# Kernel optimization log

Measured on AMD Instinct MI355X. Metric: run time of the kernel, lower is better.

## Reference

```python
import jax, jax.numpy as jnp
import numpy as np

ATOM_FDIM = 133
BOND_FDIM = 14
DIM = 512
DEPTH = 4
N_ATOMS = 100000
N_BONDS = 300000
MAX_NB = 6
N_MOLS = 500


def _lin(x, w, b):
    return x @ w + b


def setup_inputs() -> dict:
    key = jax.random.key(0)
    ks = jax.random.split(key, 16)
    s = 0.02
    f_atoms = jax.random.normal(ks[0], (N_ATOMS, ATOM_FDIM), jnp.float32)
    f_bonds = jax.random.normal(ks[1], (N_BONDS, BOND_FDIM), jnp.float32)
    a2a = jax.random.randint(ks[2], (N_ATOMS, MAX_NB), 0, N_ATOMS, jnp.int32)
    a2b = jax.random.randint(ks[3], (N_ATOMS, MAX_NB), 0, N_BONDS, jnp.int32)
    # atom 0 is padding -> assign out-of-range segment id so segment_sum drops it
    ids = np.minimum((np.arange(N_ATOMS) - 1) // ((N_ATOMS - 1) // N_MOLS), N_MOLS - 1)
    ids[0] = N_MOLS
    mol_ids = jnp.asarray(ids, jnp.int32)
    return {
        'f_atoms': f_atoms, 'f_bonds': f_bonds, 'a2a': a2a, 'a2b': a2b,
        'mol_ids': mol_ids, 'n_mols': N_MOLS,
        'W_i_w': jax.random.normal(ks[4], (ATOM_FDIM, DIM), jnp.float32) * s,
        'W_i_b': jnp.zeros((DIM,), jnp.float32),
        'Wh0_w': jax.random.normal(ks[5], (DIM + BOND_FDIM, DIM), jnp.float32) * s,
        'Wh0_b': jnp.zeros((DIM,), jnp.float32),
        'Wh1_w': jax.random.normal(ks[6], (DIM, DIM), jnp.float32) * s,
        'Wh1_b': jnp.zeros((DIM,), jnp.float32),
        'Wh2_w': jax.random.normal(ks[7], (DIM, DIM), jnp.float32) * s,
        'Wh2_b': jnp.zeros((DIM,), jnp.float32),
        'Wah0_w': jax.random.normal(ks[8], (ATOM_FDIM, DIM), jnp.float32) * s,
        'Wah0_b': jnp.zeros((DIM,), jnp.float32),
        'Wah1_w': jax.random.normal(ks[9], (DIM, DIM), jnp.float32) * s,
        'Wah1_b': jnp.zeros((DIM,), jnp.float32),
        'Wah2_w': jax.random.normal(ks[10], (DIM, DIM), jnp.float32) * s,
        'Wah2_b': jnp.zeros((DIM,), jnp.float32),
        'W_o_w': jax.random.normal(ks[11], (2 * DIM, DIM), jnp.float32) * s,
        'W_o_b': jnp.zeros((DIM,), jnp.float32),
    }


def reference(f_atoms, f_bonds, a2a, a2b, mol_ids, n_mols,
              W_i_w, W_i_b, Wh0_w, Wh0_b, Wh1_w, Wh1_b, Wh2_w, Wh2_b,
              Wah0_w, Wah0_b, Wah1_w, Wah1_b, Wah2_w, Wah2_b, W_o_w, W_o_b):
    # input atom hidden; row 0 is padding and is zeroed
    h0 = jax.nn.relu(_lin(f_atoms, W_i_w, W_i_b))        # [A, dim]
    msg = h0.at[0].set(0.0)
    self_msg = msg
    # NOTE: original code shares one modulList across all W_h{i} -> shared weights per depth
    nei_bond_sum = jnp.sum(f_bonds[a2b], axis=1)          # [A, BOND_FDIM] (constant over depths)
    for _ in range(DEPTH):
        nei_atom_sum = jnp.sum(msg[a2a], axis=1)          # [A, dim]
        m = jnp.concatenate([nei_atom_sum, nei_bond_sum], axis=1)  # [A, dim+BOND_FDIM]
        m = _lin(jax.nn.relu(m), Wh0_w, Wh0_b)
        m = _lin(jax.nn.relu(m), Wh1_w, Wh1_b)
        m = _lin(jax.nn.relu(m), Wh2_w, Wh2_b)
        m = self_msg + m
        self_msg = m                                      # kept BEFORE zeroing row 0 (as in torch)
        msg = m.at[0].set(0.0)
    a_message = jnp.sum(msg[a2a], axis=1)                 # [A, dim]
    cc = jax.nn.relu(_lin(f_atoms, Wah0_w, Wah0_b))
    cc = jax.nn.relu(_lin(cc, Wah1_w, Wah1_b))
    cc = jax.nn.relu(_lin(cc, Wah2_w, Wah2_b))
    a_input = jnp.concatenate([cc, a_message], axis=1)    # [A, 2*dim]
    out = jax.nn.relu(_lin(a_input, W_o_w, W_o_b))        # [A, dim]
    # per-molecule sum pooling (a_scope); padding atom has id == n_mols -> dropped
    return jax.ops.segment_sum(out, mol_ids, num_segments=n_mols)
```

## Files before the change

kernel.cpp:

```cpp
#include <hip/hip_runtime.h>
#include <stdint.h>
#include <stddef.h>

typedef __attribute__((ext_vector_type(8))) _Float16 half8;
typedef __attribute__((ext_vector_type(4))) float f32x4;

__device__ __forceinline__ void gload_lds16(const void* g, void* l) {
  __builtin_amdgcn_global_load_lds(
      (const __attribute__((address_space(1))) unsigned int*)g,
      (__attribute__((address_space(3))) unsigned int*)l, 16, 0, 0);
}

enum { EPI_RELU = 0, EPI_INIT = 1, EPI_DEPTH = 2 };

template <int EPI, bool SPLIT, bool ATOMS>
__global__ __launch_bounds__(256) void gemm128(
    const void* __restrict__ A1v, int lda1,
    const _Float16* __restrict__ A2, int lda2, int ksplit,
    const _Float16* __restrict__ Bt,
    const float* __restrict__ bias,
    int M, int K,
    _Float16* __restrict__ out_h, int ldo,
    const _Float16* __restrict__ self_h,
    float* self0,
    _Float16* msg_out,
    int row0)
{
  __shared__ __align__(16) _Float16 Alds[128 * 32];
  __shared__ __align__(16) _Float16 Blds[128 * 32];

  const int t = threadIdx.x;
  const int m0 = blockIdx.x * 128;
  const int n0 = blockIdx.y * 128;

  f32x4 acc[4][4];
#pragma unroll
  for (int i = 0; i < 4; ++i)
#pragma unroll
    for (int j = 0; j < 4; ++j) acc[i][j] = (f32x4){0.f, 0.f, 0.f, 0.f};

  const int lane = t & 63;
  const int w = t >> 6;
  const int wr = (w >> 1) * 64;
  const int wc = (w & 1) * 64;
  const int l16 = lane & 15;
  const int quad = lane >> 4;

  for (int kk = 0; kk < K; kk += 32) {
    __syncthreads();
    if (ATOMS) {
      const float* Af = (const float*)A1v;
#pragma unroll
      for (int h = 0; h < 2; ++h) {
        int i = t + h * 256;
        int r = i >> 2, kg = i & 3;
        int row = m0 + r; if (row > M - 1) row = M - 1;
        int k = kk + kg * 8;
        const float* src = Af + (size_t)row * lda1;
        half8 hv;
#pragma unroll
        for (int e = 0; e < 8; ++e) {
          int kc = k + e;
          hv[e] = (_Float16)(kc < ksplit ? src[kc] : 0.f);
        }
        *(half8*)&Alds[i * 8] = hv;
      }
    } else {
      const _Float16* A1 = (const _Float16*)A1v;
#pragma unroll
      for (int h = 0; h < 2; ++h) {
        int i = t + h * 256;
        int r = i >> 2, kg = i & 3;
        int row = m0 + r; if (row > M - 1) row = M - 1;
        int k = kk + kg * 8;
        const _Float16* src;
        if (SPLIT) {
          src = (k < ksplit) ? (A1 + (size_t)row * lda1 + k)
                             : (A2 + (size_t)row * lda2 + (k - ksplit));
        } else {
          src = A1 + (size_t)row * lda1 + k;
        }
        gload_lds16(src, &Alds[i * 8]);
      }
    }
#pragma unroll
    for (int h = 0; h < 2; ++h) {
      int i = t + h * 256;
      int n = i >> 2, kg = i & 3;
      gload_lds16(Bt + (size_t)(n0 + n) * K + kk + kg * 8, &Blds[i * 8]);
    }
    __syncthreads();

    half8 af[4], bf[4];
#pragma unroll
    for (int mi = 0; mi < 4; ++mi)
      af[mi] = *(const half8*)&Alds[(wr + mi * 16 + l16) * 32 + quad * 8];
#pragma unroll
    for (int ni = 0; ni < 4; ++ni)
      bf[ni] = *(const half8*)&Blds[(wc + ni * 16 + l16) * 32 + quad * 8];
#pragma unroll
    for (int mi = 0; mi < 4; ++mi)
#pragma unroll
      for (int ni = 0; ni < 4; ++ni)
        acc[mi][ni] = __builtin_amdgcn_mfma_f32_16x16x32_f16(af[mi], bf[ni], acc[mi][ni], 0, 0, 0);
  }

#pragma unroll
  for (int mi = 0; mi < 4; ++mi) {
#pragma unroll
    for (int ni = 0; ni < 4; ++ni) {
      int col = n0 + wc + ni * 16 + l16;
      float b = bias[col];
#pragma unroll
      for (int r = 0; r < 4; ++r) {
        int row = m0 + wr + mi * 16 + quad * 4 + r;
        if (row < M) {
          float v = acc[mi][ni][r] + b;
          if (EPI == EPI_RELU) {
            v = fmaxf(v, 0.f);
            out_h[(size_t)row * ldo + col] = (_Float16)v;
          } else if (EPI == EPI_INIT) {
            v = fmaxf(v, 0.f);
            if (row == row0) { msg_out[(size_t)row * 512 + col] = (_Float16)0.f; self0[col] = 0.f; }
            else msg_out[(size_t)row * 512 + col] = (_Float16)v;
          } else {
            float self = (row == row0) ? self0[col]
                                       : (float)self_h[(size_t)row * 512 + col];
            v += self;
            if (row == row0) { self0[col] = v; msg_out[(size_t)row * 512 + col] = (_Float16)0.f; }
            else msg_out[(size_t)row * 512 + col] = (_Float16)v;
          }
        }
      }
    }
  }
}

template <bool SPLIT>
__global__ __launch_bounds__(256) void gemm_wide(
    const _Float16* __restrict__ A1, int lda1,
    const _Float16* __restrict__ A2, int lda2, int ksplit,
    const _Float16* __restrict__ Bt, const float* __restrict__ bias,
    int M, int K,
    _Float16* __restrict__ out_h)
{
  __shared__ __align__(16) _Float16 Alds[64 * 32];
  __shared__ __align__(16) _Float16 Blds[512 * 32];
  const int t = threadIdx.x;
  const int m0 = blockIdx.x * 64;
  f32x4 acc[4][8];
#pragma unroll
  for (int i = 0; i < 4; ++i)
#pragma unroll
    for (int j = 0; j < 8; ++j) acc[i][j] = (f32x4){0.f, 0.f, 0.f, 0.f};
  const int lane = t & 63;
  const int w = t >> 6;
  const int wc = w * 128;
  const int l16 = lane & 15;
  const int quad = lane >> 4;
  for (int kk = 0; kk < K; kk += 32) {
    __syncthreads();
    {
      int r = t >> 2, kg = t & 3;
      int row = m0 + r; if (row > M - 1) row = M - 1;
      int k = kk + kg * 8;
      const _Float16* src;
      if (SPLIT) {
        src = (k < ksplit) ? (A1 + (size_t)row * lda1 + k)
                           : (A2 + (size_t)row * lda2 + (k - ksplit));
      } else {
        src = A1 + (size_t)row * lda1 + k;
      }
      gload_lds16(src, &Alds[t * 8]);
    }
#pragma unroll
    for (int h = 0; h < 8; ++h) {
      int i = t + h * 256;
      int n = i >> 2, kg = i & 3;
      gload_lds16(Bt + (size_t)n * K + kk + kg * 8, &Blds[i * 8]);
    }
    __syncthreads();
    half8 af[4], bf[8];
#pragma unroll
    for (int mi = 0; mi < 4; ++mi)
      af[mi] = *(const half8*)&Alds[(mi * 16 + l16) * 32 + quad * 8];
#pragma unroll
    for (int ni = 0; ni < 8; ++ni)
      bf[ni] = *(const half8*)&Blds[(wc + ni * 16 + l16) * 32 + quad * 8];
#pragma unroll
    for (int mi = 0; mi < 4; ++mi)
#pragma unroll
      for (int ni = 0; ni < 8; ++ni)
        acc[mi][ni] = __builtin_amdgcn_mfma_f32_16x16x32_f16(af[mi], bf[ni], acc[mi][ni], 0, 0, 0);
  }
#pragma unroll
  for (int mi = 0; mi < 4; ++mi) {
#pragma unroll
    for (int ni = 0; ni < 8; ++ni) {
      int col = wc + ni * 16 + l16;
      float b = bias[col];
#pragma unroll
      for (int r = 0; r < 4; ++r) {
        int row = m0 + mi * 16 + quad * 4 + r;
        if (row < M) {
          float v = fmaxf(acc[mi][ni][r] + b, 0.f);
          out_h[(size_t)row * 512 + col] = (_Float16)v;
        }
      }
    }
  }
}

template <bool RELU>
__global__ __launch_bounds__(256) void gather_k(
    const _Float16* __restrict__ msg, const int* __restrict__ a2a,
    _Float16* __restrict__ out, int rows)
{
  int t = threadIdx.x;
  int a = blockIdx.x * 4 + (t >> 6);
  if (a >= rows) return;
  int g = t & 63;
  const _Float16* base = msg + g * 8;
  float acc[8] = {0, 0, 0, 0, 0, 0, 0, 0};
#pragma unroll
  for (int j = 0; j < 6; ++j) {
    int nb = a2a[(size_t)a * 6 + j];
    half8 v = *(const half8*)(base + (size_t)nb * 512);
#pragma unroll
    for (int e = 0; e < 8; ++e) acc[e] += (float)v[e];
  }
  half8 o;
#pragma unroll
  for (int e = 0; e < 8; ++e) {
    float x = acc[e];
    if (RELU) x = fmaxf(x, 0.f);
    o[e] = (_Float16)x;
  }
  *(half8*)(out + (size_t)a * 512 + g * 8) = o;
}

__global__ __launch_bounds__(256) void bondsum_k(
    const float* __restrict__ fb, const int* __restrict__ a2b,
    _Float16* __restrict__ bnd, int A)
{
  int idx = blockIdx.x * 256 + threadIdx.x;
  int a = idx >> 5, c = idx & 31;
  if (a >= A) return;
  float s = 0.f;
  if (c < 14) {
#pragma unroll
    for (int j = 0; j < 6; ++j) s += fb[(size_t)a2b[a * 6 + j] * 14 + c];
    s = fmaxf(s, 0.f);
  }
  bnd[(size_t)a * 32 + c] = (_Float16)s;
}

__global__ __launch_bounds__(256) void padatoms_k(
    const float* __restrict__ fa, _Float16* __restrict__ ap, int A)
{
  int idx = blockIdx.x * 256 + threadIdx.x;
  if (idx >= A * 20) return;
  int a = idx / 20, c8 = (idx - a * 20) * 8;
  const float* src = fa + (size_t)a * 133;
  half8 hv;
#pragma unroll
  for (int e = 0; e < 8; ++e) {
    int c = c8 + e;
    hv[e] = (_Float16)(c < 133 ? src[c] : 0.f);
  }
  *(half8*)(ap + (size_t)a * 160 + c8) = hv;
}

struct WJobs {
  const float* src[8];
  _Float16* dst[8];
  int K[8];
  int Kpad[8];
};
__global__ __launch_bounds__(256) void wcast_all(WJobs j) {
  int job = blockIdx.y;
  int idx = blockIdx.x * 256 + threadIdx.x;
  int Kpad = j.Kpad[job];
  if (idx >= 512 * Kpad) return;
  int n = idx / Kpad, k = idx - n * Kpad;
  float v = (k < j.K[job]) ? j.src[job][(size_t)k * 512 + n] : 0.f;
  j.dst[job][idx] = (_Float16)v;
}

__global__ __launch_bounds__(256) void fill_k(float* __restrict__ p, int n, float v) {
  int i = blockIdx.x * 256 + threadIdx.x;
  if (i < n) p[i] = v;
}

__global__ __launch_bounds__(256) void segsum_k(
    const _Float16* __restrict__ x, const int* __restrict__ mol,
    float* __restrict__ out, int A, int n_mols)
{
  int t = threadIdx.x;
  int c = t * 2;
  int a0 = blockIdx.x * 128;
  int aend = a0 + 128; if (aend > A) aend = A;
  float s0 = 0.f, s1 = 0.f;
  int cur = -1;
  for (int a = a0; a < aend; ++a) {
    int m = mol[a];
    if (m != cur) {
      if (cur >= 0 && cur < n_mols) {
        atomicAdd(&out[(size_t)cur * 512 + c], s0);
        atomicAdd(&out[(size_t)cur * 512 + c + 1], s1);
      }
      cur = m; s0 = 0.f; s1 = 0.f;
    }
    const _Float16* row = x + (size_t)a * 512 + c;
    s0 += (float)row[0];
    s1 += (float)row[1];
  }
  if (cur >= 0 && cur < n_mols) {
    atomicAdd(&out[(size_t)cur * 512 + c], s0);
    atomicAdd(&out[(size_t)cur * 512 + c + 1], s1);
  }
}

extern "C" void kernel_launch(void* const* d_in, const int* in_sizes, int n_in,
                              void* d_out, int out_size, void* d_ws, size_t ws_size,
                              hipStream_t stream) {
  const float* f_atoms = (const float*)d_in[0];
  const float* f_bonds = (const float*)d_in[1];
  const int* a2a = (const int*)d_in[2];
  const int* a2b = (const int*)d_in[3];
  const int* mol_ids = (const int*)d_in[4];
  const float* W_i_w  = (const float*)d_in[6];
  const float* W_i_b  = (const float*)d_in[7];
  const float* Wh0_w  = (const float*)d_in[8];
  const float* Wh0_b  = (const float*)d_in[9];
  const float* Wh1_w  = (const float*)d_in[10];
  const float* Wh1_b  = (const float*)d_in[11];
  const float* Wh2_w  = (const float*)d_in[12];
  const float* Wh2_b  = (const float*)d_in[13];
  const float* Wah0_w = (const float*)d_in[14];
  const float* Wah0_b = (const float*)d_in[15];
  const float* Wah1_w = (const float*)d_in[16];
  const float* Wah1_b = (const float*)d_in[17];
  const float* Wah2_w = (const float*)d_in[18];
  const float* Wah2_b = (const float*)d_in[19];
  const float* W_o_w  = (const float*)d_in[20];
  const float* W_o_b  = (const float*)d_in[21];

  const int A = in_sizes[0] / 133;
  const int n_mols = out_size / 512;

  char* ws = (char*)d_ws;
  size_t off = 0;
  auto alloc = [&](size_t bytes) -> void* {
    void* p = ws + off;
    off = (off + bytes + 255) & ~(size_t)255;
    return p;
  };
  const size_t big = (size_t)A * 512 * 2;
  _Float16* MSGA = (_Float16*)alloc(big);
  _Float16* MSGB = (_Float16*)alloc(big);
  _Float16* BND = (_Float16*)alloc((size_t)A * 32 * 2);
  _Float16* Wt_i   = (_Float16*)alloc(512 * 160 * 2);
  _Float16* Wt_h0  = (_Float16*)alloc(512 * 544 * 2);
  _Float16* Wt_h1  = (_Float16*)alloc(512 * 512 * 2);
  _Float16* Wt_h2  = (_Float16*)alloc(512 * 512 * 2);
  _Float16* Wt_ah0 = (_Float16*)alloc(512 * 160 * 2);
  _Float16* Wt_ah1 = (_Float16*)alloc(512 * 512 * 2);
  _Float16* Wt_ah2 = (_Float16*)alloc(512 * 512 * 2);
  _Float16* Wt_o   = (_Float16*)alloc(512 * 1024 * 2);
  float* SELF0 = (float*)alloc(512 * 4);
  const size_t fixed = off;

  if (ws_size < fixed) {
    fill_k<<<(out_size + 255) / 256, 256, 0, stream>>>(
        (float*)d_out, out_size, (float)(ws_size >> 20));
    return;
  }

  const size_t scratch = ws_size - fixed;
  const size_t apbytes = (size_t)A * 160 * 2;
  const bool useAp = scratch >= apbytes + 256;
  _Float16* Ap = (_Float16*)(ws + fixed);

  int crows = (int)(scratch / 2 / 1024);
  crows &= ~127;
  const int Acap = (A + 127) & ~127;
  if (crows > Acap) crows = Acap;
  const bool chunked = crows >= 2048;

  {
    WJobs j;
    j.src[0] = W_i_w;  j.dst[0] = Wt_i;   j.K[0] = 133; j.Kpad[0] = 160;
    j.src[1] = Wh0_w;  j.dst[1] = Wt_h0;  j.K[1] = 526; j.Kpad[1] = 544;
    j.src[2] = Wh1_w;  j.dst[2] = Wt_h1;  j.K[2] = 512; j.Kpad[2] = 512;
    j.src[3] = Wh2_w;  j.dst[3] = Wt_h2;  j.K[3] = 512; j.Kpad[3] = 512;
    j.src[4] = Wah0_w; j.dst[4] = Wt_ah0; j.K[4] = 133; j.Kpad[4] = 160;
    j.src[5] = Wah1_w; j.dst[5] = Wt_ah1; j.K[5] = 512; j.Kpad[5] = 512;
    j.src[6] = Wah2_w; j.dst[6] = Wt_ah2; j.K[6] = 512; j.Kpad[6] = 512;
    j.src[7] = W_o_w;  j.dst[7] = Wt_o;   j.K[7] = 1024; j.Kpad[7] = 1024;
    dim3 g((512 * 1024 + 255) / 256, 8);
    wcast_all<<<g, 256, 0, stream>>>(j);
  }
  bondsum_k<<<((A * 32) + 255) / 256, 256, 0, stream>>>(f_bonds, a2b, BND, A);

  dim3 gfull((A + 127) / 128, 4);

  if (useAp) {
    padatoms_k<<<((A * 20) + 255) / 256, 256, 0, stream>>>(f_atoms, Ap, A);
    gemm128<EPI_INIT, false, false><<<gfull, 256, 0, stream>>>(
        Ap, 160, nullptr, 0, 0, Wt_i, W_i_b, A, 160,
        nullptr, 0, nullptr, SELF0, MSGA, 0);
  } else {
    gemm128<EPI_INIT, false, true><<<gfull, 256, 0, stream>>>(
        f_atoms, 133, nullptr, 0, 133, Wt_i, W_i_b, A, 160,
        nullptr, 0, nullptr, SELF0, MSGA, 0);
  }

  if (chunked) {
    _Float16* NC = (_Float16*)(ws + fixed);
    _Float16* YC = (_Float16*)(ws + fixed + (size_t)crows * 1024);

    _Float16* MO = MSGA;
    _Float16* MN = MSGB;
    for (int d = 0; d < 4; ++d) {
      for (int r0 = 0; r0 < A; r0 += crows) {
        int rows = A - r0 < crows ? A - r0 : crows;
        dim3 gg((rows + 127) / 128, 4);
        int row0 = (r0 == 0) ? 0 : -1;
        gather_k<true><<<(rows + 3) / 4, 256, 0, stream>>>(MO, a2a + (size_t)r0 * 6, NC, rows);
        gemm128<EPI_RELU, true, false><<<gg, 256, 0, stream>>>(
            NC, 512, BND + (size_t)r0 * 32, 32, 512, Wt_h0, Wh0_b, rows, 544,
            YC, 512, nullptr, nullptr, nullptr, 0);
        gemm128<EPI_RELU, false, false><<<gg, 256, 0, stream>>>(
            YC, 512, nullptr, 0, 0, Wt_h1, Wh1_b, rows, 512,
            NC, 512, nullptr, nullptr, nullptr, 0);
        gemm128<EPI_DEPTH, false, false><<<gg, 256, 0, stream>>>(
            NC, 512, nullptr, 0, 0, Wt_h2, Wh2_b, rows, 512,
            nullptr, 0, MO + (size_t)r0 * 512, SELF0, MN + (size_t)r0 * 512, row0);
      }
      _Float16* tmp = MO; MO = MN; MN = tmp;
    }
    gather_k<false><<<(A + 3) / 4, 256, 0, stream>>>(MO, a2a, MN, A);
    if (useAp) {
      padatoms_k<<<((A * 20) + 255) / 256, 256, 0, stream>>>(f_atoms, Ap, A);
      gemm128<EPI_RELU, false, false><<<gfull, 256, 0, stream>>>(
          Ap, 160, nullptr, 0, 0, Wt_ah0, Wah0_b, A, 160,
          MO, 512, nullptr, nullptr, nullptr, 0);
    } else {
      gemm128<EPI_RELU, false, true><<<gfull, 256, 0, stream>>>(
          f_atoms, 133, nullptr, 0, 133, Wt_ah0, Wah0_b, A, 160,
          MO, 512, nullptr, nullptr, nullptr, 0);
    }
    for (int r0 = 0; r0 < A; r0 += crows) {
      int rows = A - r0 < crows ? A - r0 : crows;
      dim3 gg((rows + 127) / 128, 4);
      gemm128<EPI_RELU, false, false><<<gg, 256, 0, stream>>>(
          MO + (size_t)r0 * 512, 512, nullptr, 0, 0, Wt_ah1, Wah1_b, rows, 512,
          NC, 512, nullptr, nullptr, nullptr, 0);
      gemm128<EPI_RELU, false, false><<<gg, 256, 0, stream>>>(
          NC, 512, nullptr, 0, 0, Wt_ah2, Wah2_b, rows, 512,
          YC, 512, nullptr, nullptr, nullptr, 0);
      gemm128<EPI_RELU, true, false><<<gg, 256, 0, stream>>>(
          YC, 512, MN + (size_t)r0 * 512, 512, 512, Wt_o, W_o_b, rows, 1024,
          MO + (size_t)r0 * 512, 512, nullptr, nullptr, nullptr, 0);
    }
    fill_k<<<(out_size + 255) / 256, 256, 0, stream>>>((float*)d_out, out_size, 0.f);
    segsum_k<<<(A + 127) / 128, 256, 0, stream>>>(MO, mol_ids, (float*)d_out, A, n_mols);
  } else {
    _Float16* MSG = MSGA;
    _Float16* Y1 = MSGB;
    const int gw = (A + 63) / 64;
    const int gg = (A + 3) / 4;
    for (int d = 0; d < 4; ++d) {
      gather_k<true><<<gg, 256, 0, stream>>>(MSG, a2a, Y1, A);
      gemm_wide<true><<<gw, 256, 0, stream>>>(
          Y1, 512, BND, 32, 512, Wt_h0, Wh0_b, A, 544, Y1);
      gemm_wide<false><<<gw, 256, 0, stream>>>(
          Y1, 512, nullptr, 0, 0, Wt_h1, Wh1_b, A, 512, Y1);
      gemm128<EPI_DEPTH, false, false><<<gfull, 256, 0, stream>>>(
          Y1, 512, nullptr, 0, 0, Wt_h2, Wh2_b, A, 512,
          nullptr, 0, MSG, SELF0, MSG, 0);
    }
    gather_k<false><<<gg, 256, 0, stream>>>(MSG, a2a, Y1, A);
    gemm128<EPI_RELU, false, true><<<gfull, 256, 0, stream>>>(
        f_atoms, 133, nullptr, 0, 133, Wt_ah0, Wah0_b, A, 160,
        MSG, 512, nullptr, nullptr, nullptr, 0);
    gemm_wide<false><<<gw, 256, 0, stream>>>(
        MSG, 512, nullptr, 0, 0, Wt_ah1, Wah1_b, A, 512, MSG);
    gemm_wide<false><<<gw, 256, 0, stream>>>(
        MSG, 512, nullptr, 0, 0, Wt_ah2, Wah2_b, A, 512, MSG);
    gemm_wide<true><<<gw, 256, 0, stream>>>(
        MSG, 512, Y1, 512, 512, Wt_o, W_o_b, A, 1024, Y1);
    fill_k<<<(out_size + 255) / 256, 256, 0, stream>>>((float*)d_out, out_size, 0.f);
    segsum_k<<<(A + 127) / 128, 256, 0, stream>>>(Y1, mol_ids, (float*)d_out, A, n_mols);
  }
}
```

Baseline: 3.636 ms.

## Double GEMM K-tile to 64 with XOR-swizzled LDS and add full-buffer path

Raises the K step of the 128x128 MFMA GEMM from 32 to 64, which halves the number of barrier pairs per tile. LDS rows are XOR-swizzled to avoid bank conflicts on the wider rows. Padded K sizes become multiples of 64 (160→192, 544→576), so weights and the bond/atom buffers get more zero padding and some wasted MFMA work. A new 'full' path is taken when the workspace can hold a third full-size buffer; it runs every GEMM over all rows instead of in chunks or through gemm_wide. LDS use per block doubles, which may cut occupancy.

```diff
diff --git a/kernel.cpp b/kernel.cpp
--- a/kernel.cpp
+++ b/kernel.cpp
@@ -9,6 +9,10 @@
   __builtin_amdgcn_global_load_lds(
       (const __attribute__((address_space(1))) unsigned int*)g,
       (__attribute__((address_space(3))) unsigned int*)l, 16, 0, 0);
+}
+
+__device__ __forceinline__ int sw(int row, int c) {
+  return row * 64 + ((c ^ (row & 7)) << 3);
 }
 
 enum { EPI_RELU = 0, EPI_INIT = 1, EPI_DEPTH = 2 };
@@ -26,8 +30,8 @@
     _Float16* msg_out,
     int row0)
 {
-  __shared__ __align__(16) _Float16 Alds[128 * 32];
-  __shared__ __align__(16) _Float16 Blds[128 * 32];
+  __shared__ __align__(16) _Float16 Alds[128 * 64];
+  __shared__ __align__(16) _Float16 Blds[128 * 64];
 
   const int t = threadIdx.x;
   const int m0 = blockIdx.x * 128;
@@ -46,17 +50,17 @@
   const int l16 = lane & 15;
   const int quad = lane >> 4;
 
-  for (int kk = 0; kk < K; kk += 32) {
+  for (int kk = 0; kk < K; kk += 64) {
     __syncthreads();
-    if (ATOMS) {
-      const float* Af = (const float*)A1v;
-#pragma unroll
-      for (int h = 0; h < 2; ++h) {
-        int i = t + h * 256;
-        int r = i >> 2, kg = i & 3;
-        int row = m0 + r; if (row > M - 1) row = M - 1;
-        int k = kk + kg * 8;
-        const float* src = Af + (size_t)row * lda1;
+#pragma unroll
+    for (int h = 0; h < 4; ++h) {
+      int i = t + h * 256;
+      int r = i >> 3;
+      int kg = (i & 7) ^ (r & 7);
+      int row = m0 + r; if (row > M - 1) row = M - 1;
+      int k = kk + kg * 8;
+      if (ATOMS) {
+        const float* src = (const float*)A1v + (size_t)row * lda1;
         half8 hv;
 #pragma unroll
         for (int e = 0; e < 8; ++e) {
@@ -64,15 +68,8 @@
           hv[e] = (_Float16)(kc < ksplit ? src[kc] : 0.f);
         }
         *(half8*)&Alds[i * 8] = hv;
-      }
-    } else {
-      const _Float16* A1 = (const _Float16*)A1v;
-#pragma unroll
-      for (int h = 0; h < 2; ++h) {
-        int i = t + h * 256;
-        int r = i >> 2, kg = i & 3;
-        int row = m0 + r; if (row > M - 1) row = M - 1;
-        int k = kk + kg * 8;
+      } else {
+        const _Float16* A1 = (const _Float16*)A1v;
         const _Float16* src;
         if (SPLIT) {
           src = (k < ksplit) ? (A1 + (size_t)row * lda1 + k)
@@ -84,25 +81,32 @@
       }
     }
 #pragma unroll
-    for (int h = 0; h < 2; ++h) {
+    for (int h = 0; h < 4; ++h) {
       int i = t + h * 256;
-      int n = i >> 2, kg = i & 3;
+      int n = i >> 3;
+      int kg = (i & 7) ^ (n & 7);
       gload_lds16(Bt + (size_t)(n0 + n) * K + kk + kg * 8, &Blds[i * 8]);
     }
     __syncthreads();
 
-    half8 af[4], bf[4];
-#pragma unroll
-    for (int mi = 0; mi < 4; ++mi)
-      af[mi] = *(const half8*)&Alds[(wr + mi * 16 + l16) * 32 + quad * 8];
-#pragma unroll
-    for (int ni = 0; ni < 4; ++ni)
-      bf[ni] = *(const half8*)&Blds[(wc + ni * 16 + l16) * 32 + quad * 8];
-#pragma unroll
-    for (int mi = 0; mi < 4; ++mi)
+    half8 af[4][2], bf[4][2];
+#pragma unroll
+    for (int kh = 0; kh < 2; ++kh) {
+#pragma unroll
+      for (int mi = 0; mi < 4; ++mi)
+        af[mi][kh] = *(const half8*)&Alds[sw(wr + mi * 16 + l16, kh * 4 + quad)];
 #pragma unroll
       for (int ni = 0; ni < 4; ++ni)
-        acc[mi][ni] = __builtin_amdgcn_mfma_f32_16x16x32_f16(af[mi], bf[ni], acc[mi][ni], 0, 0, 0);
+        bf[ni][kh] = *(const half8*)&Blds[sw(wc + ni * 16 + l16, kh * 4 + quad)];
+    }
+#pragma unroll
+    for (int kh = 0; kh < 2; ++kh)
+#pragma unroll
+      for (int mi = 0; mi < 4; ++mi)
+#pragma unroll
+        for (int ni = 0; ni < 4; ++ni)
+          acc[mi][ni] = __builtin_amdgcn_mfma_f32_16x16x32_f16(
+              af[mi][kh], bf[ni][kh], acc[mi][ni], 0, 0, 0);
   }
 
 #pragma unroll
@@ -244,7 +248,7 @@
     _Float16* __restrict__ bnd, int A)
 {
   int idx = blockIdx.x * 256 + threadIdx.x;
-  int a = idx >> 5, c = idx & 31;
+  int a = idx >> 6, c = idx & 63;
   if (a >= A) return;
   float s = 0.f;
   if (c < 14) {
@@ -252,15 +256,15 @@
     for (int j = 0; j < 6; ++j) s += fb[(size_t)a2b[a * 6 + j] * 14 + c];
     s = fmaxf(s, 0.f);
   }
-  bnd[(size_t)a * 32 + c] = (_Float16)s;
+  bnd[(size_t)a * 64 + c] = (_Float16)s;
 }
 
 __global__ __launch_bounds__(256) void padatoms_k(
     const float* __restrict__ fa, _Float16* __restrict__ ap, int A)
 {
   int idx = blockIdx.x * 256 + threadIdx.x;
-  if (idx >= A * 20) return;
-  int a = idx / 20, c8 = (idx - a * 20) * 8;
+  if (idx >= A * 24) return;
+  int a = idx / 24, c8 = (idx - a * 24) * 8;
   const float* src = fa + (size_t)a * 133;
   half8 hv;
 #pragma unroll
@@ -268,7 +272,7 @@
     int c = c8 + e;
     hv[e] = (_Float16)(c < 133 ? src[c] : 0.f);
   }
-  *(half8*)(ap + (size_t)a * 160 + c8) = hv;
+  *(half8*)(ap + (size_t)a * 192 + c8) = hv;
 }
 
 struct WJobs {
@@ -357,14 +361,20 @@
     return p;
   };
   const size_t big = (size_t)A * 512 * 2;
+  const size_t bndsz = (size_t)A * 64 * 2;
+  const size_t wtsz = (size_t)(192 + 576 + 512 + 512 + 192 + 512 + 512 + 1024) * 512 * 2;
+  const size_t full_req = 3 * big + bndsz + wtsz + 4096 + 16 * 256;
+  const bool full = ws_size >= full_req;
+
   _Float16* MSGA = (_Float16*)alloc(big);
   _Float16* MSGB = (_Float16*)alloc(big);
-  _Float16* BND = (_Float16*)alloc((size_t)A * 32 * 2);
-  _Float16* Wt_i   = (_Float16*)alloc(512 * 160 * 2);
-  _Float16* Wt_h0  = (_Float16*)alloc(512 * 544 * 2);
+  _Float16* Y1 = full ? (_Float16*)alloc(big) : nullptr;
+  _Float16* BND = (_Float16*)alloc(bndsz);
+  _Float16* Wt_i   = (_Float16*)alloc(512 * 192 * 2);
+  _Float16* Wt_h0  = (_Float16*)alloc(512 * 576 * 2);
   _Float16* Wt_h1  = (_Float16*)alloc(512 * 512 * 2);
   _Float16* Wt_h2  = (_Float16*)alloc(512 * 512 * 2);
-  _Float16* Wt_ah0 = (_Float16*)alloc(512 * 160 * 2);
+  _Float16* Wt_ah0 = (_Float16*)alloc(512 * 192 * 2);
   _Float16* Wt_ah1 = (_Float16*)alloc(512 * 512 * 2);
   _Float16* Wt_ah2 = (_Float16*)alloc(512 * 512 * 2);
   _Float16* Wt_o   = (_Float16*)alloc(512 * 1024 * 2);
@@ -378,48 +388,78 @@
   }
 
   const size_t scratch = ws_size - fixed;
-  const size_t apbytes = (size_t)A * 160 * 2;
-  const bool useAp = scratch >= apbytes + 256;
-  _Float16* Ap = (_Float16*)(ws + fixed);
+  const size_t apbytes = (size_t)A * 192 * 2;
+  const bool useAp = full || scratch >= apbytes + 256;
+  _Float16* Ap = full ? Y1 : (_Float16*)(ws + fixed);
 
   int crows = (int)(scratch / 2 / 1024);
   crows &= ~127;
   const int Acap = (A + 127) & ~127;
   if (crows > Acap) crows = Acap;
-  const bool chunked = crows >= 2048;
+  const bool chunked = !full && crows >= 2048;
 
   {
     WJobs j;
-    j.src[0] = W_i_w;  j.dst[0] = Wt_i;   j.K[0] = 133; j.Kpad[0] = 160;
-    j.src[1] = Wh0_w;  j.dst[1] = Wt_h0;  j.K[1] = 526; j.Kpad[1] = 544;
-    j.src[2] = Wh1_w;  j.dst[2] = Wt_h1;  j.K[2] = 512; j.Kpad[2] = 512;
-    j.src[3] = Wh2_w;  j.dst[3] = Wt_h2;  j.K[3] = 512; j.Kpad[3] = 512;
-    j.src[4] = Wah0_w; j.dst[4] = Wt_ah0; j.K[4] = 133; j.Kpad[4] = 160;
-    j.src[5] = Wah1_w; j.dst[5] = Wt_ah1; j.K[5] = 512; j.Kpad[5] = 512;
-    j.src[6] = Wah2_w; j.dst[6] = Wt_ah2; j.K[6] = 512; j.Kpad[6] = 512;
+    j.src[0] = W_i_w;  j.dst[0] = Wt_i;   j.K[0] = 133;  j.Kpad[0] = 192;
+    j.src[1] = Wh0_w;  j.dst[1] = Wt_h0;  j.K[1] = 526;  j.Kpad[1] = 576;
+    j.src[2] = Wh1_w;  j.dst[2] = Wt_h1;  j.K[2] = 512;  j.Kpad[2] = 512;
+    j.src[3] = Wh2_w;  j.dst[3] = Wt_h2;  j.K[3] = 512;  j.Kpad[3] = 512;
+    j.src[4] = Wah0_w; j.dst[4] = Wt_ah0; j.K[4] = 133;  j.Kpad[4] = 192;
+    j.src[5] = Wah1_w; j.dst[5] = Wt_ah1; j.K[5] = 512;  j.Kpad[5] = 512;
+    j.src[6] = Wah2_w; j.dst[6] = Wt_ah2; j.K[6] = 512;  j.Kpad[6] = 512;
     j.src[7] = W_o_w;  j.dst[7] = Wt_o;   j.K[7] = 1024; j.Kpad[7] = 1024;
     dim3 g((512 * 1024 + 255) / 256, 8);
     wcast_all<<<g, 256, 0, stream>>>(j);
   }
-  bondsum_k<<<((A * 32) + 255) / 256, 256, 0, stream>>>(f_bonds, a2b, BND, A);
+  bondsum_k<<<((A * 64) + 255) / 256, 256, 0, stream>>>(f_bonds, a2b, BND, A);
 
   dim3 gfull((A + 127) / 128, 4);
 
   if (useAp) {
-    padatoms_k<<<((A * 20) + 255) / 256, 256, 0, stream>>>(f_atoms, Ap, A);
+    padatoms_k<<<((A * 24) + 255) / 256, 256, 0, stream>>>(f_atoms, Ap, A);
     gemm128<EPI_INIT, false, false><<<gfull, 256, 0, stream>>>(
-        Ap, 160, nullptr, 0, 0, Wt_i, W_i_b, A, 160,
+        Ap, 192, nullptr, 0, 0, Wt_i, W_i_b, A, 192,
         nullptr, 0, nullptr, SELF0, MSGA, 0);
   } else {
     gemm128<EPI_INIT, false, true><<<gfull, 256, 0, stream>>>(
-        f_atoms, 133, nullptr, 0, 133, Wt_i, W_i_b, A, 160,
+        f_atoms, 133, nullptr, 0, 133, Wt_i, W_i_b, A, 192,
         nullptr, 0, nullptr, SELF0, MSGA, 0);
   }
 
-  if (chunked) {
+  if (full) {
+    _Float16* MSG = MSGA;
+    _Float16* NEI = MSGB;
+    for (int d = 0; d < 4; ++d) {
+      gather_k<true><<<(A + 3) / 4, 256, 0, stream>>>(MSG, a2a, NEI, A);
+      gemm128<EPI_RELU, true, false><<<gfull, 256, 0, stream>>>(
+          NEI, 512, BND, 64, 512, Wt_h0, Wh0_b, A, 576,
+          Y1, 512, nullptr, nullptr, nullptr, 0);
+      gemm128<EPI_RELU, false, false><<<gfull, 256, 0, stream>>>(
+          Y1, 512, nullptr, 0, 0, Wt_h1, Wh1_b, A, 512,
+          NEI, 512, nullptr, nullptr, nullptr, 0);
+      gemm128<EPI_DEPTH, false, false><<<gfull, 256, 0, stream>>>(
+          NEI, 512, nullptr, 0, 0, Wt_h2, Wh2_b, A, 512,
+          nullptr, 0, MSG, SELF0, MSG, 0);
+    }
+    gather_k<false><<<(A + 3) / 4, 256, 0, stream>>>(MSG, a2a, NEI, A);
+    padatoms_k<<<((A * 24) + 255) / 256, 256, 0, stream>>>(f_atoms, Ap, A);
+    gemm128<EPI_RELU, false, false><<<gfull, 256, 0, stream>>>(
+        Ap, 192, nullptr, 0, 0, Wt_ah0, Wah0_b, A, 192,
+        MSG, 512, nullptr, nullptr, nullptr, 0);
+    gemm128<EPI_RELU, false, false><<<gfull, 256, 0, stream>>>(
+        MSG, 512, nullptr, 0, 0, Wt_ah1, Wah1_b, A, 512,
+        Y1, 512, nullptr, nullptr, nullptr, 0);
+    gemm128<EPI_RELU, false, false><<<gfull, 256, 0, stream>>>(
+        Y1, 512, nullptr, 0, 0, Wt_ah2, Wah2_b, A, 512,
+        MSG, 512, nullptr, nullptr, nullptr, 0);
+    gemm128<EPI_RELU, true, false><<<gfull, 256, 0, stream>>>(
+        MSG, 512, NEI, 512, 512, Wt_o, W_o_b, A, 1024,
+        Y1, 512, nullptr, nullptr, nullptr, 0);
+    fill_k<<<(out_size + 255) / 256, 256, 0, stream>>>((float*)d_out, out_size, 0.f);
+    segsum_k<<<(A + 127) / 128, 256, 0, stream>>>(Y1, mol_ids, (float*)d_out, A, n_mols);
+  } else if (chunked) {
     _Float16* NC = (_Float16*)(ws + fixed);
     _Float16* YC = (_Float16*)(ws + fixed + (size_t)crows * 1024);
-
     _Float16* MO = MSGA;
     _Float16* MN = MSGB;
     for (int d = 0; d < 4; ++d) {
@@ -429,7 +469,7 @@
         int row0 = (r0 == 0) ? 0 : -1;
         gather_k<true><<<(rows + 3) / 4, 256, 0, stream>>>(MO, a2a + (size_t)r0 * 6, NC, rows);
         gemm128<EPI_RELU, true, false><<<gg, 256, 0, stream>>>(
-            NC, 512, BND + (size_t)r0 * 32, 32, 512, Wt_h0, Wh0_b, rows, 544,
+            NC, 512, BND + (size_t)r0 * 64, 64, 512, Wt_h0, Wh0_b, rows, 576,
             YC, 512, nullptr, nullptr, nullptr, 0);
         gemm128<EPI_RELU, false, false><<<gg, 256, 0, stream>>>(
             YC, 512, nullptr, 0, 0, Wt_h1, Wh1_b, rows, 512,
@@ -442,13 +482,13 @@
     }
     gather_k<false><<<(A + 3) / 4, 256, 0, stream>>>(MO, a2a, MN, A);
     if (useAp) {
-      padatoms_k<<<((A * 20) + 255) / 256, 256, 0, stream>>>(f_atoms, Ap, A);
+      padatoms_k<<<((A * 24) + 255) / 256, 256, 0, stream>>>(f_atoms, Ap, A);
       gemm128<EPI_RELU, false, false><<<gfull, 256, 0, stream>>>(
-          Ap, 160, nullptr, 0, 0, Wt_ah0, Wah0_b, A, 160,
+          Ap, 192, nullptr, 0, 0, Wt_ah0, Wah0_b, A, 192,
           MO, 512, nullptr, nullptr, nullptr, 0);
     } else {
       gemm128<EPI_RELU, false, true><<<gfull, 256, 0, stream>>>(
-          f_atoms, 133, nullptr, 0, 133, Wt_ah0, Wah0_b, A, 160,
+          f_atoms, 133, nullptr, 0, 133, Wt_ah0, Wah0_b, A, 192,
           MO, 512, nullptr, nullptr, nullptr, 0);
     }
     for (int r0 = 0; r0 < A; r0 += crows) {
@@ -468,30 +508,30 @@
     segsum_k<<<(A + 127) / 128, 256, 0, stream>>>(MO, mol_ids, (float*)d_out, A, n_mols);
   } else {
     _Float16* MSG = MSGA;
-    _Float16* Y1 = MSGB;
+    _Float16* Y1b = MSGB;
     const int gw = (A + 63) / 64;
     const int gg = (A + 3) / 4;
     for (int d = 0; d < 4; ++d) {
-      gather_k<true><<<gg, 256, 0, stream>>>(MSG, a2a, Y1, A);
+      gather_k<true><<<gg, 256, 0, stream>>>(MSG, a2a, Y1b, A);
       gemm_wide<true><<<gw, 256, 0, stream>>>(
-          Y1, 512, BND, 32, 512, Wt_h0, Wh0_b, A, 544, Y1);
+          Y1b, 512, BND, 64, 512, Wt_h0, Wh0_b, A, 576, Y1b);
       gemm_wide<false><<<gw, 256, 0, stream>>>(
-          Y1, 512, nullptr, 0, 0, Wt_h1, Wh1_b, A, 512, Y1);
+          Y1b, 512, nullptr, 0, 0, Wt_h1, Wh1_b, A, 512, Y1b);
       gemm128<EPI_DEPTH, false, false><<<gfull, 256, 0, stream>>>(
-          Y1, 512, nullptr, 0, 0, Wt_h2, Wh2_b, A, 512,
+          Y1b, 512, nullptr, 0, 0, Wt_h2, Wh2_b, A, 512,
           nullptr, 0, MSG, SELF0, MSG, 0);
     }
-    gather_k<false><<<gg, 256, 0, stream>>>(MSG, a2a, Y1, A);
+    gather_k<false><<<gg, 256, 0, stream>>>(MSG, a2a, Y1b, A);
     gemm128<EPI_RELU, false, true><<<gfull, 256, 0, stream>>>(
-        f_atoms, 133, nullptr, 0, 133, Wt_ah0, Wah0_b, A, 160,
+        f_atoms, 133, nullptr, 0, 133, Wt_ah0, Wah0_b, A, 192,
         MSG, 512, nullptr, nullptr, nullptr, 0);
     gemm_wide<false><<<gw, 256, 0, stream>>>(
         MSG, 512, nullptr, 0, 0, Wt_ah1, Wah1_b, A, 512, MSG);
     gemm_wide<false><<<gw, 256, 0, stream>>>(
         MSG, 512, nullptr, 0, 0, Wt_ah2, Wah2_b, A, 512, MSG);
     gemm_wide<true><<<gw, 256, 0, stream>>>(
-        MSG, 512, Y1, 512, 512, Wt_o, W_o_b, A, 1024, Y1);
+        MSG, 512, Y1b, 512, 512, Wt_o, W_o_b, A, 1024, Y1b);
     fill_k<<<(out_size + 255) / 256, 256, 0, stream>>>((float*)d_out, out_size, 0.f);
-    segsum_k<<<(A + 127) / 128, 256, 0, stream>>>(Y1, mol_ids, (float*)d_out, A, n_mols);
-  }
-}
+    segsum_k<<<(A + 127) / 128, 256, 0, stream>>>(Y1b, mol_ids, (float*)d_out, A, n_mols);
+  }
+}
```

Result: faster. 3.359 ms (-7.6%).
